# Kernel tuning notes

Measured on AMD Instinct MI355X. Metric: run time of the kernel, lower is better.

Reference implementation:

```python
import jax, jax.numpy as jnp
import numpy as np

N_GRAPHS = 128
N_NODES = 512
N = N_GRAPHS * N_NODES      # 65536 total nodes
E = 524288                  # edges (avg degree 8)
F_IN = 4                    # num_features
EMB = 4                     # embedding_dim
HEADS = 4
GDIM = 16                   # GATConv_dim
D = GDIM * HEADS            # 64 = d_model
NHEAD = 2                   # heads // 2
FF = 64                     # ff_hid_dim
OUT = 64                    # output_dim
N_GAT_REST = 3              # gat_layers - 1


def setup_inputs() -> dict:
    key = jax.random.key(0)
    ks = iter(jax.random.split(key, 64))
    def nrm(shape, fan_in):
        return jax.random.normal(next(ks), shape, jnp.float32) / np.float32(np.sqrt(fan_in))
    inp = {}
    inp['x'] = jax.random.normal(next(ks), (N, F_IN), jnp.float32)
    inp['edge_index'] = jax.random.randint(next(ks), (2, E), 0, N, dtype=jnp.int32)
    inp['batch'] = jnp.repeat(jnp.arange(N_GRAPHS, dtype=jnp.int32), N_NODES)
    # feature_fc
    inp['Wf'] = nrm((F_IN, EMB), F_IN); inp['bf'] = jnp.zeros((EMB,), jnp.float32)
    # input GATConv (EMB -> HEADS*GDIM)
    inp['gW0'] = nrm((EMB, HEADS * GDIM), EMB)
    inp['aS0'] = nrm((HEADS, GDIM), GDIM); inp['aD0'] = nrm((HEADS, GDIM), GDIM)
    inp['gb0'] = jnp.zeros((D,), jnp.float32)
    # remaining 3 GATConv layers (D -> HEADS*GDIM), stacked
    inp['gW'] = nrm((N_GAT_REST, D, HEADS * GDIM), D)
    inp['aS'] = nrm((N_GAT_REST, HEADS, GDIM), GDIM); inp['aD'] = nrm((N_GAT_REST, HEADS, GDIM), GDIM)
    inp['gb'] = jnp.zeros((N_GAT_REST, D), jnp.float32)
    # decoder layer: self-attn, cross-attn, layernorms, FFN
    for p in ['sWq','sWk','sWv','sWo','cWq','cWk','cWv','cWo']:
        inp[p] = nrm((D, D), D)
    for p in ['sbq','sbk','sbv','sbo','cbq','cbk','cbv','cbo']:
        inp[p] = jnp.zeros((D,), jnp.float32)
    for g, b in [('ln1g','ln1b'), ('ln2g','ln2b'), ('ln3g','ln3b')]:
        inp[g] = jnp.ones((D,), jnp.float32); inp[b] = jnp.zeros((D,), jnp.float32)
    inp['ffW1'] = nrm((D, FF), D); inp['ffb1'] = jnp.zeros((FF,), jnp.float32)
    inp['ffW2'] = nrm((FF, D), FF); inp['ffb2'] = jnp.zeros((D,), jnp.float32)
    inp['fcW'] = nrm((D, OUT), D); inp['fcb'] = jnp.zeros((OUT,), jnp.float32)
    return inp


def _gat(h_in, src, dst, W, a_s, a_d, b):
    # PyG GATConv, concat=True, negative_slope=0.2, self-loops already in (src,dst)
    h = (h_in @ W).reshape(N, HEADS, GDIM)
    es = jnp.einsum('nho,ho->nh', h, a_s)   # [N,H]
    ed = jnp.einsum('nho,ho->nh', h, a_d)
    e = jax.nn.leaky_relu(es[src] + ed[dst], 0.2)          # [E',H]
    m = jax.ops.segment_max(e, dst, num_segments=N)        # segment softmax over dst
    w = jnp.exp(e - m[dst])
    s = jax.ops.segment_sum(w, dst, num_segments=N)
    alpha = w / (s[dst] + 1e-16)
    out = jax.ops.segment_sum(h[src] * alpha[..., None], dst, num_segments=N)
    return out.reshape(N, D) + b


def _mha(q, kv, Wq, bq, Wk, bk, Wv, bv, Wo, bo):
    B, S, Dm = q.shape
    hd = Dm // NHEAD
    Q = (q @ Wq + bq).reshape(B, S, NHEAD, hd)
    K = (kv @ Wk + bk).reshape(B, S, NHEAD, hd)
    V = (kv @ Wv + bv).reshape(B, S, NHEAD, hd)
    a = jax.nn.softmax(jnp.einsum('bqhd,bkhd->bhqk', Q, K) / jnp.sqrt(jnp.float32(hd)), axis=-1)
    o = jnp.einsum('bhqk,bkhd->bqhd', a, V).reshape(B, S, Dm)
    return o @ Wo + bo


def _ln(x, g, b):
    m = x.mean(-1, keepdims=True)
    v = ((x - m) ** 2).mean(-1, keepdims=True)
    return (x - m) / jnp.sqrt(v + 1e-5) * g + b


def reference(x, edge_index, batch, Wf, bf, gW0, aS0, aD0, gb0, gW, aS, aD, gb,
              sWq, sWk, sWv, sWo, cWq, cWk, cWv, cWo,
              sbq, sbk, sbv, sbo, cbq, cbk, cbv, cbo,
              ln1g, ln1b, ln2g, ln2b, ln3g, ln3b,
              ffW1, ffb1, ffW2, ffb2, fcW, fcb):
    loops = jnp.arange(N, dtype=edge_index.dtype)
    src = jnp.concatenate([edge_index[0], loops])
    dst = jnp.concatenate([edge_index[1], loops])
    h = x @ Wf + bf
    h = jax.nn.leaky_relu(_gat(h, src, dst, gW0, aS0, aD0, gb0), 0.01)
    for i in range(N_GAT_REST):
        h = jax.nn.leaky_relu(_gat(h, src, dst, gW[i], aS[i], aD[i], gb[i]), 0.01)
    t = h.reshape(N_GRAPHS, N_NODES, D)
    # one transformer decoder layer, post-norm, memory = layer input
    mem = t
    t = _ln(t + _mha(t, t, sWq, sbq, sWk, sbk, sWv, sbv, sWo, sbo), ln1g, ln1b)
    t = _ln(t + _mha(t, mem, cWq, cbq, cWk, cbk, cWv, cbv, cWo, cbo), ln2g, ln2b)
    t = _ln(t + (jax.nn.relu(t @ ffW1 + ffb1) @ ffW2 + ffb2), ln3g, ln3b)
    h = t.reshape(N, D)
    pooled = jax.ops.segment_sum(h, batch, num_segments=N_GRAPHS) / jnp.float32(N_NODES)
    return pooled @ fcW + fcb
```

## Files before the change

### kernel.cpp

```cpp
#include <hip/hip_runtime.h>
#include <math.h>

#define NG 128
#define SEQ 512
#define NN 65536
#define EE 524288
#define DM 64
#define HSTR 80

typedef __attribute__((ext_vector_type(8))) short short8;
typedef __attribute__((ext_vector_type(4))) float f32x4;

__device__ __forceinline__ float lrelu(float x, float s){ return x > 0.f ? x : s*x; }

__device__ __forceinline__ unsigned short f2bf(float x){
  union { float f; unsigned u; } v; v.f = x;
  unsigned r = v.u + 0x7FFF + ((v.u>>16)&1);
  return (unsigned short)(r>>16);
}
__device__ __forceinline__ float bf2f(unsigned short x){
  union { unsigned u; float f; } v; v.u = ((unsigned)x)<<16;
  return v.f;
}

__global__ void k_count(const int* __restrict__ dst, int* __restrict__ deg){
  int e = blockIdx.x*256 + threadIdx.x;
  atomicAdd(&deg[dst[e]], 1);
}

__global__ void k_scan1(const int* __restrict__ deg, int* __restrict__ excl, int* __restrict__ bsums){
  __shared__ int sm[256];
  int tid = threadIdx.x;
  int i = blockIdx.x*256 + tid;
  int v = deg[i];
  sm[tid] = v;
  __syncthreads();
  int val = v;
  for (int off=1; off<256; off<<=1){
    int add = (tid>=off)? sm[tid-off] : 0;
    __syncthreads();
    val += add;
    sm[tid] = val;
    __syncthreads();
  }
  excl[i] = val - v;
  if (tid==255) bsums[blockIdx.x] = val;
}

__global__ void k_scan2(int* __restrict__ bsums){
  __shared__ int sm[256];
  int tid=threadIdx.x;
  int v = bsums[tid];
  sm[tid]=v;
  __syncthreads();
  int val=v;
  for (int off=1; off<256; off<<=1){
    int add = (tid>=off)? sm[tid-off]:0;
    __syncthreads();
    val += add;
    sm[tid]=val;
    __syncthreads();
  }
  bsums[tid] = val - v;
}

__global__ void k_scan3(const int* __restrict__ excl, const int* __restrict__ bsums,
                        int* __restrict__ rowp, int* __restrict__ cursor){
  int i = blockIdx.x*256 + threadIdx.x;
  int v = excl[i] + bsums[blockIdx.x];
  rowp[i]=v; cursor[i]=v;
  if (i==0) rowp[NN]=EE;
}

__global__ void k_fill(const int* __restrict__ src, const int* __restrict__ dst,
                       int* __restrict__ cursor, int* __restrict__ col){
  int e = blockIdx.x*256 + threadIdx.x;
  int d = dst[e];
  int p = atomicAdd(&cursor[d], 1);
  col[p] = src[e];
}

__global__ void __launch_bounds__(256) k_transform0(const float* __restrict__ x,
                            const float* __restrict__ Wf, const float* __restrict__ bf,
                            const float* __restrict__ gW0,
                            const float* __restrict__ aSp, const float* __restrict__ aDp,
                            unsigned short* __restrict__ hout, float* __restrict__ ed){
  __shared__ float inL[4][68];
  __shared__ float Wl[4][64];
  __shared__ float b0l[64];
  __shared__ float asl[64], adl[64];
  int tid = threadIdx.x;
  int n0 = blockIdx.x*64;
  if (tid < 64){
    asl[tid] = aSp[tid]; adl[tid] = aDp[tid];
    float b = 0.f;
    #pragma unroll
    for (int k=0;k<4;k++) b += bf[k]*gW0[k*64+tid];
    b0l[tid] = b;
  }
  {
    int i = tid>>6, j = tid&63;
    float s = 0.f;
    #pragma unroll
    for (int k=0;k<4;k++) s += Wf[i*4+k]*gW0[k*64+j];
    Wl[i][j] = s;
  }
  if (tid < 64){
    float4 v = *(const float4*)&x[(size_t)(n0+tid)*4];
    inL[0][tid]=v.x; inL[1][tid]=v.y; inL[2][tid]=v.z; inL[3][tid]=v.w;
  }
  __syncthreads();
  int i = tid>>4, j = tid&15;
  float acc[4][4];
  #pragma unroll
  for (int r=0;r<4;r++){
    #pragma unroll
    for (int c=0;c<4;c++) acc[r][c] = 0.f;
  }
  #pragma unroll
  for (int k=0;k<4;k++){
    float4 av = *(float4*)&inL[k][4*i];
    float4 bv = *(float4*)&Wl[k][4*j];
    float a_[4]={av.x,av.y,av.z,av.w}, b_[4]={bv.x,bv.y,bv.z,bv.w};
    #pragma unroll
    for (int r=0;r<4;r++){
      #pragma unroll
      for (int c=0;c<4;c++) acc[r][c] += a_[r]*b_[c];
    }
  }
  float4 asv = *(float4*)&asl[4*j];
  float4 adv = *(float4*)&adl[4*j];
  float4 bbv = *(float4*)&b0l[4*j];
  float bb[4] = {bbv.x, bbv.y, bbv.z, bbv.w};
  #pragma unroll
  for (int r=0;r<4;r++){
    float y0=acc[r][0]+bb[0], y1=acc[r][1]+bb[1], y2=acc[r][2]+bb[2], y3=acc[r][3]+bb[3];
    int node = n0 + 4*i + r;
    ushort4 hv;
    hv.x=f2bf(y0); hv.y=f2bf(y1); hv.z=f2bf(y2); hv.w=f2bf(y3);
    *(ushort4*)&hout[(size_t)node*HSTR + 4*j] = hv;
    float ps = y0*asv.x + y1*asv.y + y2*asv.z + y3*asv.w;
    float pd = y0*adv.x + y1*adv.y + y2*adv.z + y3*adv.w;
    ps += __shfl_xor(ps,1); ps += __shfl_xor(ps,2);
    pd += __shfl_xor(pd,1); pd += __shfl_xor(pd,2);
    if ((j&3)==0){
      *(float*)&hout[(size_t)node*HSTR + 64 + 2*(j>>2)] = ps;
      ed[(size_t)node*4 + (j>>2)] = pd;
    }
  }
}

__global__ void __launch_bounds__(256) k_transform_bf(const unsigned short* __restrict__ hin, const float* __restrict__ W,
                            const float* __restrict__ aSp, const float* __restrict__ aDp,
                            unsigned short* __restrict__ hout, float* __restrict__ ed){
  __shared__ float inL[64][68];
  __shared__ float Wl[64][64];
  __shared__ float asl[64], adl[64];
  int tid = threadIdx.x;
  int n0 = blockIdx.x*64;
  if (tid < 64){ asl[tid] = aSp[tid]; adl[tid] = aDp[tid]; }
  for (int idx=tid; idx<1024; idx+=256){
    int k = idx>>4, jj = (idx&15)<<2;
    *(float4*)&Wl[k][jj] = *(const float4*)&W[k*64+jj];
  }
  for (int idx=tid; idx<1024; idx+=256){
    int node = idx>>4, kk = (idx&15)<<2;
    ushort4 v = *(const ushort4*)&hin[(size_t)(n0+node)*64 + kk];
    inL[kk][node]=bf2f(v.x); inL[kk+1][node]=bf2f(v.y); inL[kk+2][node]=bf2f(v.z); inL[kk+3][node]=bf2f(v.w);
  }
  __syncthreads();
  int i = tid>>4, j = tid&15;
  float acc[4][4];
  #pragma unroll
  for (int r=0;r<4;r++){
    #pragma unroll
    for (int c=0;c<4;c++) acc[r][c] = 0.f;
  }
  #pragma unroll 4
  for (int k=0;k<64;k++){
    float4 av = *(float4*)&inL[k][4*i];
    float4 bv = *(float4*)&Wl[k][4*j];
    float a_[4]={av.x,av.y,av.z,av.w}, b_[4]={bv.x,bv.y,bv.z,bv.w};
    #pragma unroll
    for (int r=0;r<4;r++){
      #pragma unroll
      for (int c=0;c<4;c++) acc[r][c] += a_[r]*b_[c];
    }
  }
  float4 asv = *(float4*)&asl[4*j];
  float4 adv = *(float4*)&adl[4*j];
  #pragma unroll
  for (int r=0;r<4;r++){
    float y0=acc[r][0], y1=acc[r][1], y2=acc[r][2], y3=acc[r][3];
    int node = n0 + 4*i + r;
    ushort4 hv;
    hv.x=f2bf(y0); hv.y=f2bf(y1); hv.z=f2bf(y2); hv.w=f2bf(y3);
    *(ushort4*)&hout[(size_t)node*HSTR + 4*j] = hv;
    float ps = y0*asv.x + y1*asv.y + y2*asv.z + y3*asv.w;
    float pd = y0*adv.x + y1*adv.y + y2*adv.z + y3*adv.w;
    ps += __shfl_xor(ps,1); ps += __shfl_xor(ps,2);
    pd += __shfl_xor(pd,1); pd += __shfl_xor(pd,2);
    if ((j&3)==0){
      *(float*)&hout[(size_t)node*HSTR + 64 + 2*(j>>2)] = ps;
      ed[(size_t)node*4 + (j>>2)] = pd;
    }
  }
}

template<int BF16OUT>
__global__ void __launch_bounds__(256) k_aggregate(const unsigned short* __restrict__ h,
                            const float* __restrict__ ed, const int* __restrict__ rowp,
                            const int* __restrict__ col, const float* __restrict__ gb,
                            void* __restrict__ houtv){
  int tid = threadIdx.x;
  int n = blockIdx.x*4 + (tid>>6);
  int l = tid&63;
  int q = l>>4;
  int sl = l&15;
  int head = sl>>2;
  float edn = ed[(size_t)n*4 + head];
  float es_self = *(const float*)&h[(size_t)n*HSTR + 64 + 2*head];
  int beg = __builtin_amdgcn_readfirstlane(rowp[n]);
  int end = __builtin_amdgcn_readfirstlane(rowp[n+1]);
  float m = -1e30f, s = 0.f;
  float a0=0.f, a1=0.f, a2=0.f, a3=0.f;
  int i = beg;
  for (; i+8 <= end; i += 8){
    int c0=col[i], c1=col[i+1], c2=col[i+2], c3=col[i+3];
    int c4=col[i+4], c5=col[i+5], c6=col[i+6], c7=col[i+7];
    int t01 = (q&1)? c1 : c0;
    int t23 = (q&1)? c3 : c2;
    int sq0 = (q&2)? t23 : t01;
    int t45 = (q&1)? c5 : c4;
    int t67 = (q&1)? c7 : c6;
    int sq1 = (q&2)? t67 : t45;
    size_t b0r = (size_t)sq0*HSTR, b1r = (size_t)sq1*HSTR;
    ushort4 hv0 = *(const ushort4*)&h[b0r + 4*sl];
    ushort4 hv1 = *(const ushort4*)&h[b1r + 4*sl];
    float e0 = lrelu(*(const float*)&h[b0r + 64 + 2*head] + edn, 0.2f);
    float e1 = lrelu(*(const float*)&h[b1r + 64 + 2*head] + edn, 0.2f);
    float mx = fmaxf(e0, e1);
    if (__any(mx > m + 8.f)){
      float nm = fmaxf(m, mx);
      float c = __expf(m - nm);
      s*=c; a0*=c; a1*=c; a2*=c; a3*=c; m = nm;
    }
    float w0 = __expf(e0 - m);
    float w1 = __expf(e1 - m);
    s += w0 + w1;
    a0 += w0*bf2f(hv0.x) + w1*bf2f(hv1.x);
    a1 += w0*bf2f(hv0.y) + w1*bf2f(hv1.y);
    a2 += w0*bf2f(hv0.z) + w1*bf2f(hv1.z);
    a3 += w0*bf2f(hv0.w) + w1*bf2f(hv1.w);
  }
  if (i < end){
    int last = end-1;
    int i1=(i+1<last)?i+1:last, i2=(i+2<last)?i+2:last, i3=(i+3<last)?i+3:last;
    int i4=(i+4<last)?i+4:last, i5=(i+5<last)?i+5:last, i6=(i+6<last)?i+6:last;
    int c0=col[i], c1=col[i1], c2=col[i2], c3=col[i3];
    int c4=col[i4], c5=col[i5], c6=col[i6], c7=col[last];
    int t01 = (q&1)? c1 : c0;
    int t23 = (q&1)? c3 : c2;
    int sq0 = (q&2)? t23 : t01;
    int t45 = (q&1)? c5 : c4;
    int t67 = (q&1)? c7 : c6;
    int sq1 = (q&2)? t67 : t45;
    bool ac0 = (i + q) < end;
    bool ac1 = (i + 4 + q) < end;
    size_t b0r = (size_t)sq0*HSTR, b1r = (size_t)sq1*HSTR;
    ushort4 hv0 = *(const ushort4*)&h[b0r + 4*sl];
    ushort4 hv1 = *(const ushort4*)&h[b1r + 4*sl];
    float e0 = lrelu(*(const float*)&h[b0r + 64 + 2*head] + edn, 0.2f);
    float e1 = lrelu(*(const float*)&h[b1r + 64 + 2*head] + edn, 0.2f);
    if (!ac0) e0 = -1e30f;
    if (!ac1) e1 = -1e30f;
    float mx = fmaxf(e0, e1);
    if (__any(mx > m + 8.f)){
      float nm = fmaxf(m, mx);
      float c = __expf(m - nm);
      s*=c; a0*=c; a1*=c; a2*=c; a3*=c; m = nm;
    }
    float w0 = ac0 ? __expf(e0 - m) : 0.f;
    float w1 = ac1 ? __expf(e1 - m) : 0.f;
    s += w0 + w1;
    a0 += w0*bf2f(hv0.x) + w1*bf2f(hv1.x);
    a1 += w0*bf2f(hv0.y) + w1*bf2f(hv1.y);
    a2 += w0*bf2f(hv0.z) + w1*bf2f(hv1.z);
    a3 += w0*bf2f(hv0.w) + w1*bf2f(hv1.w);
  }
  #pragma unroll
  for (int off=16; off<=32; off<<=1){
    float m2 = __shfl_xor(m, off);
    float s2 = __shfl_xor(s, off);
    float b0 = __shfl_xor(a0, off);
    float b1 = __shfl_xor(a1, off);
    float b2 = __shfl_xor(a2, off);
    float b3 = __shfl_xor(a3, off);
    float nm = fmaxf(m, m2);
    float c1 = __expf(m - nm), c2 = __expf(m2 - nm);
    s  = s*c1  + s2*c2;
    a0 = a0*c1 + b0*c2;
    a1 = a1*c1 + b1*c2;
    a2 = a2*c1 + b2*c2;
    a3 = a3*c1 + b3*c2;
    m = nm;
  }
  {
    float e_self = lrelu(es_self + edn, 0.2f);
    float nm = fmaxf(m, e_self);
    float c = __expf(m - nm), cs = __expf(e_self - nm);
    ushort4 hs = *(const ushort4*)&h[(size_t)n*HSTR + 4*sl];
    s  = s*c  + cs;
    a0 = a0*c + cs*bf2f(hs.x);
    a1 = a1*c + cs*bf2f(hs.y);
    a2 = a2*c + cs*bf2f(hs.z);
    a3 = a3*c + cs*bf2f(hs.w);
  }
  if (q == 0){
    float inv = 1.f/(s + 1e-16f);
    float4 gv = *(const float4*)&gb[4*sl];
    float o0 = lrelu(a0*inv + gv.x, 0.01f);
    float o1 = lrelu(a1*inv + gv.y, 0.01f);
    float o2 = lrelu(a2*inv + gv.z, 0.01f);
    float o3 = lrelu(a3*inv + gv.w, 0.01f);
    if (BF16OUT){
      ushort4 hv; hv.x=f2bf(o0); hv.y=f2bf(o1); hv.z=f2bf(o2); hv.w=f2bf(o3);
      *(ushort4*)((unsigned short*)houtv + (size_t)n*64 + 4*sl) = hv;
    } else {
      *(float4*)((float*)houtv + (size_t)n*64 + 4*sl) = make_float4(o0,o1,o2,o3);
    }
  }
}

__global__ void __launch_bounds__(256) k_qkv3(const float* __restrict__ in0, const float* __restrict__ W0, const float* __restrict__ b0, unsigned short* __restrict__ o0,
                      const float* __restrict__ in1, const float* __restrict__ W1, const float* __restrict__ b1, unsigned short* __restrict__ o1,
                      const float* __restrict__ in2, const float* __restrict__ W2, const float* __restrict__ b2, unsigned short* __restrict__ o2,
                      float scl0){
  __shared__ float inL[64][68];
  __shared__ float Wl[64][64];
  int tid = threadIdx.x;
  int n0 = blockIdx.x*64;
  int i = tid>>4, j = tid&15;
  const float* ins[3] = {in0, in1, in2};
  const float* Ws[3] = {W0, W1, W2};
  const float* bs[3] = {b0, b1, b2};
  unsigned short* os[3] = {o0, o1, o2};
  const float* cur = nullptr;
  for (int w=0; w<3; w++){
    __syncthreads();
    if (ins[w] != cur){
      cur = ins[w];
      for (int idx=tid; idx<1024; idx+=256){
        int node = idx>>4, kk = (idx&15)<<2;
        float4 v = *(const float4*)&cur[(size_t)(n0+node)*64 + kk];
        inL[kk][node]=v.x; inL[kk+1][node]=v.y; inL[kk+2][node]=v.z; inL[kk+3][node]=v.w;
      }
    }
    for (int idx=tid; idx<1024; idx+=256){
      int k = idx>>4, jj = (idx&15)<<2;
      *(float4*)&Wl[k][jj] = *(const float4*)&Ws[w][k*64+jj];
    }
    __syncthreads();
    float acc[4][4];
    #pragma unroll
    for (int r=0;r<4;r++){
      #pragma unroll
      for (int c=0;c<4;c++) acc[r][c] = 0.f;
    }
    #pragma unroll 4
    for (int k=0;k<64;k++){
      float4 av = *(float4*)&inL[k][4*i];
      float4 bv = *(float4*)&Wl[k][4*j];
      float a_[4]={av.x,av.y,av.z,av.w}, b_[4]={bv.x,bv.y,bv.z,bv.w};
      #pragma unroll
      for (int r=0;r<4;r++){
        #pragma unroll
        for (int c=0;c<4;c++) acc[r][c] += a_[r]*b_[c];
      }
    }
    float4 bv = *(const float4*)&bs[w][4*j];
    float bb[4] = {bv.x, bv.y, bv.z, bv.w};
    float sc = (w==0) ? scl0 : 1.f;
    #pragma unroll
    for (int r=0;r<4;r++){
      ushort4 hv;
      hv.x = f2bf((acc[r][0]+bb[0])*sc);
      hv.y = f2bf((acc[r][1]+bb[1])*sc);
      hv.z = f2bf((acc[r][2]+bb[2])*sc);
      hv.w = f2bf((acc[r][3]+bb[3])*sc);
      *(ushort4*)&os[w][(size_t)(n0+4*i+r)*64 + 4*j] = hv;
    }
  }
}

__global__ void __launch_bounds__(256) k_resln_bf(const unsigned short* __restrict__ in, const float* __restrict__ W,
                               const float* __restrict__ b, const float* __restrict__ res,
                               const float* __restrict__ g, const float* __restrict__ bl,
                               float* __restrict__ out){
  __shared__ float inL[64][68];
  __shared__ float Wl[64][64];
  int tid = threadIdx.x;
  int n0 = blockIdx.x*64;
  for (int idx=tid; idx<1024; idx+=256){
    int k = idx>>4, jj = (idx&15)<<2;
    *(float4*)&Wl[k][jj] = *(const float4*)&W[k*64+jj];
  }
  for (int idx=tid; idx<1024; idx+=256){
    int node = idx>>4, kk = (idx&15)<<2;
    ushort4 v = *(const ushort4*)&in[(size_t)(n0+node)*64 + kk];
    inL[kk][node]=bf2f(v.x); inL[kk+1][node]=bf2f(v.y); inL[kk+2][node]=bf2f(v.z); inL[kk+3][node]=bf2f(v.w);
  }
  __syncthreads();
  int i = tid>>4, j = tid&15;
  float acc[4][4];
  #pragma unroll
  for (int r=0;r<4;r++){
    #pragma unroll
    for (int c=0;c<4;c++) acc[r][c] = 0.f;
  }
  #pragma unroll 4
  for (int k=0;k<64;k++){
    float4 av = *(float4*)&inL[k][4*i];
    float4 bv = *(float4*)&Wl[k][4*j];
    float a_[4]={av.x,av.y,av.z,av.w}, b_[4]={bv.x,bv.y,bv.z,bv.w};
    #pragma unroll
    for (int r=0;r<4;r++){
      #pragma unroll
      for (int c=0;c<4;c++) acc[r][c] += a_[r]*b_[c];
    }
  }
  float4 bv = *(const float4*)&b[4*j];
  float bb[4] = {bv.x, bv.y, bv.z, bv.w};
  float4 gv = *(const float4*)&g[4*j];
  float4 blv = *(const float4*)&bl[4*j];
  float gg[4] = {gv.x, gv.y, gv.z, gv.w};
  float bb2[4] = {blv.x, blv.y, blv.z, blv.w};
  #pragma unroll
  for (int r=0;r<4;r++){
    int node = n0 + 4*i + r;
    float4 rv = *(const float4*)&res[(size_t)node*64 + 4*j];
    float y[4] = {acc[r][0]+bb[0]+rv.x, acc[r][1]+bb[1]+rv.y,
                  acc[r][2]+bb[2]+rv.z, acc[r][3]+bb[3]+rv.w};
    float s = (y[0]+y[1]) + (y[2]+y[3]);
    s += __shfl_xor(s,1); s += __shfl_xor(s,2); s += __shfl_xor(s,4); s += __shfl_xor(s,8);
    float mean = s * (1.f/64.f);
    float d[4] = {y[0]-mean, y[1]-mean, y[2]-mean, y[3]-mean};
    float v = (d[0]*d[0]+d[1]*d[1]) + (d[2]*d[2]+d[3]*d[3]);
    v += __shfl_xor(v,1); v += __shfl_xor(v,2); v += __shfl_xor(v,4); v += __shfl_xor(v,8);
    float inv = rsqrtf(v*(1.f/64.f) + 1e-5f);
    *(float4*)&out[(size_t)node*64 + 4*j] =
      make_float4(d[0]*inv*gg[0]+bb2[0], d[1]*inv*gg[1]+bb2[1],
                  d[2]*inv*gg[2]+bb2[2], d[3]*inv*gg[3]+bb2[3]);
  }
}

__global__ void __launch_bounds__(256) k_ffn(const float* __restrict__ in,
                     const float* __restrict__ W1p, const float* __restrict__ b1p,
                     const float* __restrict__ W2p, const float* __restrict__ b2p,
                     const float* __restrict__ g, const float* __restrict__ bl,
                     float* __restrict__ out){
  __shared__ float inL[64][68];
  __shared__ float Wl[64][64];
  __shared__ float ffL[64][68];
  int tid = threadIdx.x;
  int n0 = blockIdx.x*64;
  for (int idx=tid; idx<1024; idx+=256){
    int k = idx>>4, jj = (idx&15)<<2;
    *(float4*)&Wl[k][jj] = *(const float4*)&W1p[k*64+jj];
  }
  for (int idx=tid; idx<1024; idx+=256){
    int node = idx>>4, kk = (idx&15)<<2;
    float4 v = *(const float4*)&in[(size_t)(n0+node)*64 + kk];
    inL[kk][node]=v.x; inL[kk+1][node]=v.y; inL[kk+2][node]=v.z; inL[kk+3][node]=v.w;
  }
  __syncthreads();
  int i = tid>>4, j = tid&15;
  float acc[4][4];
  #pragma unroll
  for (int r=0;r<4;r++){
    #pragma unroll
    for (int c=0;c<4;c++) acc[r][c] = 0.f;
  }
  #pragma unroll 4
  for (int k=0;k<64;k++){
    float4 av = *(float4*)&inL[k][4*i];
    float4 bv = *(float4*)&Wl[k][4*j];
    float a_[4]={av.x,av.y,av.z,av.w}, b_[4]={bv.x,bv.y,bv.z,bv.w};
    #pragma unroll
    for (int r=0;r<4;r++){
      #pragma unroll
      for (int c=0;c<4;c++) acc[r][c] += a_[r]*b_[c];
    }
  }
  float4 b1v = *(const float4*)&b1p[4*j];
  float bb1[4] = {b1v.x, b1v.y, b1v.z, b1v.w};
  #pragma unroll
  for (int r=0;r<4;r++){
    #pragma unroll
    for (int c=0;c<4;c++){
      ffL[4*j+c][4*i+r] = fmaxf(acc[r][c] + bb1[c], 0.f);
    }
  }
  __syncthreads();
  for (int idx=tid; idx<1024; idx+=256){
    int k = idx>>4, jj = (idx&15)<<2;
    *(float4*)&Wl[k][jj] = *(const float4*)&W2p[k*64+jj];
  }
  __syncthreads();
  #pragma unroll
  for (int r=0;r<4;r++){
    #pragma unroll
    for (int c=0;c<4;c++) acc[r][c] = 0.f;
  }
  #pragma unroll 4
  for (int k=0;k<64;k++){
    float4 av = *(float4*)&ffL[k][4*i];
    float4 bv = *(float4*)&Wl[k][4*j];
    float a_[4]={av.x,av.y,av.z,av.w}, b_[4]={bv.x,bv.y,bv.z,bv.w};
    #pragma unroll
    for (int r=0;r<4;r++){
      #pragma unroll
      for (int c=0;c<4;c++) acc[r][c] += a_[r]*b_[c];
    }
  }
  float4 b2v = *(const float4*)&b2p[4*j];
  float bb2v[4] = {b2v.x, b2v.y, b2v.z, b2v.w};
  float4 gv = *(const float4*)&g[4*j];
  float4 blv = *(const float4*)&bl[4*j];
  float gg[4] = {gv.x, gv.y, gv.z, gv.w};
  float bbl[4] = {blv.x, blv.y, blv.z, blv.w};
  #pragma unroll
  for (int r=0;r<4;r++){
    int node = n0 + 4*i + r;
    float y[4];
    #pragma unroll
    for (int c=0;c<4;c++) y[c] = acc[r][c] + bb2v[c] + inL[4*j+c][4*i+r];
    float s = (y[0]+y[1]) + (y[2]+y[3]);
    s += __shfl_xor(s,1); s += __shfl_xor(s,2); s += __shfl_xor(s,4); s += __shfl_xor(s,8);
    float mean = s * (1.f/64.f);
    float d[4] = {y[0]-mean, y[1]-mean, y[2]-mean, y[3]-mean};
    float v = (d[0]*d[0]+d[1]*d[1]) + (d[2]*d[2]+d[3]*d[3]);
    v += __shfl_xor(v,1); v += __shfl_xor(v,2); v += __shfl_xor(v,4); v += __shfl_xor(v,8);
    float inv = rsqrtf(v*(1.f/64.f) + 1e-5f);
    *(float4*)&out[(size_t)node*64 + 4*j] =
      make_float4(d[0]*inv*gg[0]+bbl[0], d[1]*inv*gg[1]+bbl[1],
                  d[2]*inv*gg[2]+bbl[2], d[3]*inv*gg[3]+bbl[3]);
  }
}

__global__ void __launch_bounds__(512, 4) k_attn(const unsigned short* __restrict__ Q, const unsigned short* __restrict__ K,
                      const unsigned short* __restrict__ V, unsigned short* __restrict__ Out){
  __shared__ char smem[40960];
  char* Ksm = smem;
  char* Vsm = smem + 16384;
  char* Psm = smem + 32768;

  int bid = blockIdx.x;
  int qh = bid & 1;
  int h  = (bid>>1) & 1;
  int b  = bid>>2;
  int tid = threadIdx.x;
  int wave = tid>>6;
  int l = tid & 63;
  int lq = l & 15;
  int g  = l >> 4;
  const size_t hb = (size_t)b*SEQ*64 + (size_t)h*32;
  const f32x4 zero = {0.f,0.f,0.f,0.f};

  int qbase = qh*256 + wave*32;
  short8 qf[2];
  f32x4 O[2][2];
  float m_[2], l_[2];
  #pragma unroll
  for (int qt=0; qt<2; qt++){
    qf[qt] = *(const short8*)(Q + hb + (size_t)(qbase + qt*16 + lq)*64 + g*8);
    O[qt][0] = zero; O[qt][1] = zero;
    m_[qt] = -1e30f; l_[qt] = 0.f;
  }

  char* Pw = Psm + wave*1024;

  for (int ph=0; ph<2; ph++){
    __syncthreads();
    #pragma unroll
    for (int it=0; it<2; it++){
      int i = tid + it*512;
      int row = i>>2, j = i&3;
      uint4 v = *(const uint4*)(K + hb + (size_t)(ph*256 + row)*64 + j*8);
      *(uint4*)(Ksm + row*64 + ((j*16) ^ (((row>>1)&3)<<4))) = v;
    }
    #pragma unroll
    for (int it=0; it<2; it++){
      int i = tid + it*512;
      int key = i>>2, j = i&3;
      uint4 vv = *(const uint4*)(V + hb + (size_t)(ph*256 + key)*64 + j*8);
      const unsigned short* vs = (const unsigned short*)&vv;
      #pragma unroll
      for (int c=0;c<8;c++){
        int d = j*8 + c;
        *(unsigned short*)(Vsm + d*512 + ((key*2) ^ ((d&7)<<4))) = vs[c];
      }
    }
    __syncthreads();
    for (int p=0; p<8; p++){
      int r0 = p*32 + lq, r1 = r0 + 16;
      short8 kf0 = *(short8*)(Ksm + r0*64 + ((g*16) ^ (((r0>>1)&3)<<4)));
      short8 kf1 = *(short8*)(Ksm + r1*64 + ((g*16) ^ (((r1>>1)&3)<<4)));
      int d0 = lq, d1 = lq + 16;
      short8 vt0 = *(short8*)(Vsm + d0*512 + ((p*64 + g*16) ^ ((d0&7)<<4)));
      short8 vt1 = *(short8*)(Vsm + d1*512 + ((p*64 + g*16) ^ ((d1&7)<<4)));
      int swzp = ((lq>>1)&3)<<4;
      #pragma unroll
      for (int qt=0; qt<2; qt++){
        f32x4 s0 = __builtin_amdgcn_mfma_f32_16x16x32_bf16(kf0, qf[qt], zero, 0,0,0);
        f32x4 s1 = __builtin_amdgcn_mfma_f32_16x16x32_bf16(kf1, qf[qt], zero, 0,0,0);
        float pmax = fmaxf(fmaxf(fmaxf(s0.x,s0.y),fmaxf(s0.z,s0.w)),
                           fmaxf(fmaxf(s1.x,s1.y),fmaxf(s1.z,s1.w)));
        pmax = fmaxf(pmax, __shfl_xor(pmax, 16));
        pmax = fmaxf(pmax, __shfl_xor(pmax, 32));
        float mn = fmaxf(m_[qt], pmax);
        float corr = __expf(m_[qt] - mn);
        m_[qt] = mn;
        float e0 = __expf(s0.x - mn), e1 = __expf(s0.y - mn);
        float e2 = __expf(s0.z - mn), e3 = __expf(s0.w - mn);
        float e4 = __expf(s1.x - mn), e5 = __expf(s1.y - mn);
        float e6 = __expf(s1.z - mn), e7 = __expf(s1.w - mn);
        l_[qt] = l_[qt]*corr + (((e0+e1)+(e2+e3)) + ((e4+e5)+(e6+e7)));
        O[qt][0] *= corr; O[qt][1] *= corr;
        uint2 w0, w1;
        w0.x = (unsigned)f2bf(e0) | ((unsigned)f2bf(e1)<<16);
        w0.y = (unsigned)f2bf(e2) | ((unsigned)f2bf(e3)<<16);
        w1.x = (unsigned)f2bf(e4) | ((unsigned)f2bf(e5)<<16);
        w1.y = (unsigned)f2bf(e6) | ((unsigned)f2bf(e7)<<16);
        *(uint2*)(Pw + lq*64 + ((g*8) ^ swzp)) = w0;
        *(uint2*)(Pw + lq*64 + ((32 + g*8) ^ swzp)) = w1;
        short8 pb = *(short8*)(Pw + lq*64 + ((g*16) ^ swzp));
        O[qt][0] = __builtin_amdgcn_mfma_f32_16x16x32_bf16(vt0, pb, O[qt][0], 0,0,0);
        O[qt][1] = __builtin_amdgcn_mfma_f32_16x16x32_bf16(vt1, pb, O[qt][1], 0,0,0);
      }
    }
  }
  #pragma unroll
  for (int qt=0; qt<2; qt++){
    float lt = l_[qt];
    lt += __shfl_xor(lt, 16);
    lt += __shfl_xor(lt, 32);
    float inv = 1.f/lt;
    unsigned short* op = Out + hb + (size_t)(qbase + qt*16 + lq)*64;
    ushort4 o0, o1;
    o0.x=f2bf(O[qt][0].x*inv); o0.y=f2bf(O[qt][0].y*inv); o0.z=f2bf(O[qt][0].z*inv); o0.w=f2bf(O[qt][0].w*inv);
    o1.x=f2bf(O[qt][1].x*inv); o1.y=f2bf(O[qt][1].y*inv); o1.z=f2bf(O[qt][1].z*inv); o1.w=f2bf(O[qt][1].w*inv);
    *(ushort4*)(op + g*4) = o0;
    *(ushort4*)(op + 16 + g*4) = o1;
  }
}

__global__ void __launch_bounds__(256) k_pool_fc(const float* __restrict__ t, const float* __restrict__ fcW,
                          const float* __restrict__ fcb, float* __restrict__ out){
  __shared__ float pl[4][64];
  __shared__ float pf[64];
  int b = blockIdx.x;
  int tid = threadIdx.x;
  int j = tid&63, seg = tid>>6;
  const float* basep = t + (size_t)b*SEQ*64;
  float s = 0.f;
  for (int si=seg*128; si<(seg+1)*128; si++) s += basep[(size_t)si*64 + j];
  pl[seg][j] = s;
  __syncthreads();
  if (tid < 64){
    pf[tid] = (pl[0][tid]+pl[1][tid]+pl[2][tid]+pl[3][tid]) * (1.f/512.f);
  }
  __syncthreads();
  if (tid < 64){
    float o = fcb[tid];
    for (int k=0;k<64;k++) o += pf[k]*fcW[k*64+tid];
    out[(size_t)b*64 + tid] = o;
  }
}

extern "C" void kernel_launch(void* const* d_in, const int* in_sizes, int n_in,
                              void* d_out, int out_size, void* d_ws, size_t ws_size,
                              hipStream_t stream) {
  const float* x    = (const float*)d_in[0];
  const int*   ei   = (const int*)d_in[1];
  const float* Wf   = (const float*)d_in[3];
  const float* bf   = (const float*)d_in[4];
  const float* gW0  = (const float*)d_in[5];
  const float* aS0  = (const float*)d_in[6];
  const float* aD0  = (const float*)d_in[7];
  const float* gb0  = (const float*)d_in[8];
  const float* gW   = (const float*)d_in[9];
  const float* aS   = (const float*)d_in[10];
  const float* aD   = (const float*)d_in[11];
  const float* gb   = (const float*)d_in[12];
  const float* sWq  = (const float*)d_in[13];
  const float* sWk  = (const float*)d_in[14];
  const float* sWv  = (const float*)d_in[15];
  const float* sWo  = (const float*)d_in[16];
  const float* cWq  = (const float*)d_in[17];
  const float* cWk  = (const float*)d_in[18];
  const float* cWv  = (const float*)d_in[19];
  const float* cWo  = (const float*)d_in[20];
  const float* sbq  = (const float*)d_in[21];
  const float* sbk  = (const float*)d_in[22];
  const float* sbv  = (const float*)d_in[23];
  const float* sbo  = (const float*)d_in[24];
  const float* cbq  = (const float*)d_in[25];
  const float* cbk  = (const float*)d_in[26];
  const float* cbv  = (const float*)d_in[27];
  const float* cbo  = (const float*)d_in[28];
  const float* ln1g = (const float*)d_in[29];
  const float* ln1b = (const float*)d_in[30];
  const float* ln2g = (const float*)d_in[31];
  const float* ln2b = (const float*)d_in[32];
  const float* ln3g = (const float*)d_in[33];
  const float* ln3b = (const float*)d_in[34];
  const float* ffW1 = (const float*)d_in[35];
  const float* ffb1 = (const float*)d_in[36];
  const float* ffW2 = (const float*)d_in[37];
  const float* ffb2 = (const float*)d_in[38];
  const float* fcW  = (const float*)d_in[39];
  const float* fcb  = (const float*)d_in[40];

  char* ws = (char*)d_ws;
  size_t off = 0;
  auto alloc = [&](size_t bytes) -> void* {
    void* p = ws + off;
    off += (bytes + 255) & ~(size_t)255;
    return p;
  };
  int* deg    = (int*)alloc(NN*sizeof(int));
  int* excl   = (int*)alloc(NN*sizeof(int));
  int* rowp   = (int*)alloc((NN+1)*sizeof(int));
  int* cursor = (int*)alloc(NN*sizeof(int));
  int* col    = (int*)alloc(EE*sizeof(int));
  int* bsums  = (int*)alloc(256*sizeof(int));
  float* ed   = (float*)alloc((size_t)NN*4*sizeof(float));
  unsigned short* Hb   = (unsigned short*)alloc((size_t)NN*HSTR*sizeof(unsigned short));
  unsigned short* Hagg = (unsigned short*)alloc((size_t)NN*64*sizeof(unsigned short));
  unsigned short* Qb = (unsigned short*)alloc((size_t)NN*64*sizeof(unsigned short));
  unsigned short* Kb = (unsigned short*)alloc((size_t)NN*64*sizeof(unsigned short));
  unsigned short* Vb = (unsigned short*)alloc((size_t)NN*64*sizeof(unsigned short));
  unsigned short* Ob = (unsigned short*)alloc((size_t)NN*64*sizeof(unsigned short));
  float* B1   = (float*)alloc((size_t)NN*64*sizeof(float));
  float* B2   = (float*)alloc((size_t)NN*64*sizeof(float));
  float* B5   = (float*)alloc((size_t)NN*64*sizeof(float));

  const int* e_src = ei;
  const int* e_dst = ei + EE;

  const float scale = 0.17677669529663687f;

  hipMemsetAsync(deg, 0, NN*sizeof(int), stream);
  k_count<<<EE/256, 256, 0, stream>>>(e_dst, deg);
  k_scan1<<<NN/256, 256, 0, stream>>>(deg, excl, bsums);
  k_scan2<<<1, 256, 0, stream>>>(bsums);
  k_scan3<<<NN/256, 256, 0, stream>>>(excl, bsums, rowp, cursor);
  k_fill<<<EE/256, 256, 0, stream>>>(e_src, e_dst, cursor, col);

  k_transform0<<<NN/64, 256, 0, stream>>>(x, Wf, bf, gW0, aS0, aD0, Hb, ed);
  k_aggregate<1><<<NN/4, 256, 0, stream>>>(Hb, ed, rowp, col, gb0, Hagg);
  k_transform_bf<<<NN/64, 256, 0, stream>>>(Hagg, gW+0*4096, aS+0*64, aD+0*64, Hb, ed);
  k_aggregate<1><<<NN/4, 256, 0, stream>>>(Hb, ed, rowp, col, gb+0*64, Hagg);
  k_transform_bf<<<NN/64, 256, 0, stream>>>(Hagg, gW+1*4096, aS+1*64, aD+1*64, Hb, ed);
  k_aggregate<1><<<NN/4, 256, 0, stream>>>(Hb, ed, rowp, col, gb+1*64, Hagg);
  k_transform_bf<<<NN/64, 256, 0, stream>>>(Hagg, gW+2*4096, aS+2*64, aD+2*64, Hb, ed);
  k_aggregate<0><<<NN/4, 256, 0, stream>>>(Hb, ed, rowp, col, gb+2*64, B2);

  k_qkv3<<<NN/64, 256, 0, stream>>>(B2, sWq, sbq, Qb, B2, sWk, sbk, Kb, B2, sWv, sbv, Vb, scale);
  k_attn<<<NG*2*2, 512, 0, stream>>>(Qb, Kb, Vb, Ob);
  k_resln_bf<<<NN/64, 256, 0, stream>>>(Ob, sWo, sbo, B2, ln1g, ln1b, B5);

  k_qkv3<<<NN/64, 256, 0, stream>>>(B5, cWq, cbq, Qb, B2, cWk, cbk, Kb, B2, cWv, cbv, Vb, scale);
  k_attn<<<NG*2*2, 512, 0, stream>>>(Qb, Kb, Vb, Ob);
  k_resln_bf<<<NN/64, 256, 0, stream>>>(Ob, cWo, cbo, B5, ln2g, ln2b, B2);

  k_ffn<<<NN/64, 256, 0, stream>>>(B2, ffW1, ffb1, ffW2, ffb2, ln3g, ln3b, B1);

  k_pool_fc<<<NG, 256, 0, stream>>>(B1, fcW, fcb, (float*)d_out);
}
```

Measured before the change: 412.1 us.

## Fuse attention with output projection, residual and layernorm per half-graph block

Merges the attention kernel and the output-projection plus residual-LayerNorm kernel into one. Each block now covers both heads for 256 query rows, so the normalized attention output is staged in shared memory and multiplied by Wo there instead of being written to and re-read from global memory. This removes the Ob buffer round trip and one launch per attention stage. In exchange the grid halves to 256 blocks, shared memory per block grows, and the launch-bounds occupancy hint is dropped, which may reduce parallelism on a large GPU.

```diff
diff --git a/kernel.cpp b/kernel.cpp
--- a/kernel.cpp
+++ b/kernel.cpp
@@ -393,67 +393,6 @@
   }
 }
 
-__global__ void __launch_bounds__(256) k_resln_bf(const unsigned short* __restrict__ in, const float* __restrict__ W,
-                               const float* __restrict__ b, const float* __restrict__ res,
-                               const float* __restrict__ g, const float* __restrict__ bl,
-                               float* __restrict__ out){
-  __shared__ float inL[64][68];
-  __shared__ float Wl[64][64];
-  int tid = threadIdx.x;
-  int n0 = blockIdx.x*64;
-  for (int idx=tid; idx<1024; idx+=256){
-    int k = idx>>4, jj = (idx&15)<<2;
-    *(float4*)&Wl[k][jj] = *(const float4*)&W[k*64+jj];
-  }
-  for (int idx=tid; idx<1024; idx+=256){
-    int node = idx>>4, kk = (idx&15)<<2;
-    ushort4 v = *(const ushort4*)&in[(size_t)(n0+node)*64 + kk];
-    inL[kk][node]=bf2f(v.x); inL[kk+1][node]=bf2f(v.y); inL[kk+2][node]=bf2f(v.z); inL[kk+3][node]=bf2f(v.w);
-  }
-  __syncthreads();
-  int i = tid>>4, j = tid&15;
-  float acc[4][4];
-  #pragma unroll
-  for (int r=0;r<4;r++){
-    #pragma unroll
-    for (int c=0;c<4;c++) acc[r][c] = 0.f;
-  }
-  #pragma unroll 4
-  for (int k=0;k<64;k++){
-    float4 av = *(float4*)&inL[k][4*i];
-    float4 bv = *(float4*)&Wl[k][4*j];
-    float a_[4]={av.x,av.y,av.z,av.w}, b_[4]={bv.x,bv.y,bv.z,bv.w};
-    #pragma unroll
-    for (int r=0;r<4;r++){
-      #pragma unroll
-      for (int c=0;c<4;c++) acc[r][c] += a_[r]*b_[c];
-    }
-  }
-  float4 bv = *(const float4*)&b[4*j];
-  float bb[4] = {bv.x, bv.y, bv.z, bv.w};
-  float4 gv = *(const float4*)&g[4*j];
-  float4 blv = *(const float4*)&bl[4*j];
-  float gg[4] = {gv.x, gv.y, gv.z, gv.w};
-  float bb2[4] = {blv.x, blv.y, blv.z, blv.w};
-  #pragma unroll
-  for (int r=0;r<4;r++){
-    int node = n0 + 4*i + r;
-    float4 rv = *(const float4*)&res[(size_t)node*64 + 4*j];
-    float y[4] = {acc[r][0]+bb[0]+rv.x, acc[r][1]+bb[1]+rv.y,
-                  acc[r][2]+bb[2]+rv.z, acc[r][3]+bb[3]+rv.w};
-    float s = (y[0]+y[1]) + (y[2]+y[3]);
-    s += __shfl_xor(s,1); s += __shfl_xor(s,2); s += __shfl_xor(s,4); s += __shfl_xor(s,8);
-    float mean = s * (1.f/64.f);
-    float d[4] = {y[0]-mean, y[1]-mean, y[2]-mean, y[3]-mean};
-    float v = (d[0]*d[0]+d[1]*d[1]) + (d[2]*d[2]+d[3]*d[3]);
-    v += __shfl_xor(v,1); v += __shfl_xor(v,2); v += __shfl_xor(v,4); v += __shfl_xor(v,8);
-    float inv = rsqrtf(v*(1.f/64.f) + 1e-5f);
-    *(float4*)&out[(size_t)node*64 + 4*j] =
-      make_float4(d[0]*inv*gg[0]+bb2[0], d[1]*inv*gg[1]+bb2[1],
-                  d[2]*inv*gg[2]+bb2[2], d[3]*inv*gg[3]+bb2[3]);
-  }
-}
-
 __global__ void __launch_bounds__(256) k_ffn(const float* __restrict__ in,
                      const float* __restrict__ W1p, const float* __restrict__ b1p,
                      const float* __restrict__ W2p, const float* __restrict__ b2p,
@@ -548,70 +487,74 @@
   }
 }
 
-__global__ void __launch_bounds__(512, 4) k_attn(const unsigned short* __restrict__ Q, const unsigned short* __restrict__ K,
-                      const unsigned short* __restrict__ V, unsigned short* __restrict__ Out){
-  __shared__ char smem[40960];
+__global__ void __launch_bounds__(512) k_attn_fused(const unsigned short* __restrict__ Q, const unsigned short* __restrict__ K,
+                      const unsigned short* __restrict__ V,
+                      const float* __restrict__ Wo, const float* __restrict__ bo,
+                      const float* __restrict__ res, const float* __restrict__ g, const float* __restrict__ bl,
+                      float* __restrict__ out){
+  __shared__ __align__(16) char smem[52224];
   char* Ksm = smem;
   char* Vsm = smem + 16384;
   char* Psm = smem + 32768;
 
   int bid = blockIdx.x;
   int qh = bid & 1;
-  int h  = (bid>>1) & 1;
-  int b  = bid>>2;
+  int b  = bid >> 1;
   int tid = threadIdx.x;
   int wave = tid>>6;
   int l = tid & 63;
   int lq = l & 15;
-  int g  = l >> 4;
-  const size_t hb = (size_t)b*SEQ*64 + (size_t)h*32;
+  int g4 = l >> 4;
+  int head = wave & 1;
+  int qg = wave >> 1;
+  const size_t gb = (size_t)b*SEQ*64;
+  const int hoff = head*32;
   const f32x4 zero = {0.f,0.f,0.f,0.f};
 
-  int qbase = qh*256 + wave*32;
-  short8 qf[2];
-  f32x4 O[2][2];
-  float m_[2], l_[2];
-  #pragma unroll
-  for (int qt=0; qt<2; qt++){
-    qf[qt] = *(const short8*)(Q + hb + (size_t)(qbase + qt*16 + lq)*64 + g*8);
+  int qrow0 = qh*256 + qg*64;
+  short8 qf[4];
+  f32x4 O[4][2];
+  float m_[4], l_[4];
+  #pragma unroll
+  for (int qt=0; qt<4; qt++){
+    qf[qt] = *(const short8*)(Q + gb + (size_t)(qrow0 + qt*16 + lq)*64 + hoff + g4*8);
     O[qt][0] = zero; O[qt][1] = zero;
     m_[qt] = -1e30f; l_[qt] = 0.f;
   }
-
   char* Pw = Psm + wave*1024;
 
-  for (int ph=0; ph<2; ph++){
+  for (int ph=0; ph<4; ph++){
     __syncthreads();
     #pragma unroll
     for (int it=0; it<2; it++){
-      int i = tid + it*512;
-      int row = i>>2, j = i&3;
-      uint4 v = *(const uint4*)(K + hb + (size_t)(ph*256 + row)*64 + j*8);
-      *(uint4*)(Ksm + row*64 + ((j*16) ^ (((row>>1)&3)<<4))) = v;
+      int idx = tid + it*512;
+      int row = idx>>3, gr = idx&7;
+      uint4 v = *(const uint4*)(K + gb + (size_t)(ph*128 + row)*64 + gr*8);
+      *(uint4*)(Ksm + row*128 + ((gr*16) ^ ((row&7)<<4))) = v;
     }
     #pragma unroll
     for (int it=0; it<2; it++){
-      int i = tid + it*512;
-      int key = i>>2, j = i&3;
-      uint4 vv = *(const uint4*)(V + hb + (size_t)(ph*256 + key)*64 + j*8);
+      int idx = tid + it*512;
+      int key = idx>>3, gr = idx&7;
+      uint4 vv = *(const uint4*)(V + gb + (size_t)(ph*128 + key)*64 + gr*8);
       const unsigned short* vs = (const unsigned short*)&vv;
       #pragma unroll
       for (int c=0;c<8;c++){
-        int d = j*8 + c;
-        *(unsigned short*)(Vsm + d*512 + ((key*2) ^ ((d&7)<<4))) = vs[c];
+        int d = gr*8 + c;
+        *(unsigned short*)(Vsm + d*256 + ((key*2) ^ ((d&7)<<4))) = vs[c];
       }
     }
     __syncthreads();
-    for (int p=0; p<8; p++){
+    for (int p=0; p<4; p++){
       int r0 = p*32 + lq, r1 = r0 + 16;
-      short8 kf0 = *(short8*)(Ksm + r0*64 + ((g*16) ^ (((r0>>1)&3)<<4)));
-      short8 kf1 = *(short8*)(Ksm + r1*64 + ((g*16) ^ (((r1>>1)&3)<<4)));
-      int d0 = lq, d1 = lq + 16;
-      short8 vt0 = *(short8*)(Vsm + d0*512 + ((p*64 + g*16) ^ ((d0&7)<<4)));
-      short8 vt1 = *(short8*)(Vsm + d1*512 + ((p*64 + g*16) ^ ((d1&7)<<4)));
+      short8 kf0 = *(short8*)(Ksm + r0*128 + ((hoff*2 + g4*16) ^ ((r0&7)<<4)));
+      short8 kf1 = *(short8*)(Ksm + r1*128 + ((hoff*2 + g4*16) ^ ((r1&7)<<4)));
+      int d0 = hoff + lq, d1 = hoff + lq + 16;
+      short8 vt0 = *(short8*)(Vsm + d0*256 + ((p*64 + g4*16) ^ ((d0&7)<<4)));
+      short8 vt1 = *(short8*)(Vsm + d1*256 + ((p*64 + g4*16) ^ ((d1&7)<<4)));
       int swzp = ((lq>>1)&3)<<4;
       #pragma unroll
-      for (int qt=0; qt<2; qt++){
+      for (int qt=0; qt<4; qt++){
         f32x4 s0 = __builtin_amdgcn_mfma_f32_16x16x32_bf16(kf0, qf[qt], zero, 0,0,0);
         f32x4 s1 = __builtin_amdgcn_mfma_f32_16x16x32_bf16(kf1, qf[qt], zero, 0,0,0);
         float pmax = fmaxf(fmaxf(fmaxf(s0.x,s0.y),fmaxf(s0.z,s0.w)),
@@ -632,26 +575,77 @@
         w0.y = (unsigned)f2bf(e2) | ((unsigned)f2bf(e3)<<16);
         w1.x = (unsigned)f2bf(e4) | ((unsigned)f2bf(e5)<<16);
         w1.y = (unsigned)f2bf(e6) | ((unsigned)f2bf(e7)<<16);
-        *(uint2*)(Pw + lq*64 + ((g*8) ^ swzp)) = w0;
-        *(uint2*)(Pw + lq*64 + ((32 + g*8) ^ swzp)) = w1;
-        short8 pb = *(short8*)(Pw + lq*64 + ((g*16) ^ swzp));
+        *(uint2*)(Pw + lq*64 + ((g4*8) ^ swzp)) = w0;
+        *(uint2*)(Pw + lq*64 + ((32 + g4*8) ^ swzp)) = w1;
+        short8 pb = *(short8*)(Pw + lq*64 + ((g4*16) ^ swzp));
         O[qt][0] = __builtin_amdgcn_mfma_f32_16x16x32_bf16(vt0, pb, O[qt][0], 0,0,0);
         O[qt][1] = __builtin_amdgcn_mfma_f32_16x16x32_bf16(vt1, pb, O[qt][1], 0,0,0);
       }
     }
   }
-  #pragma unroll
-  for (int qt=0; qt<2; qt++){
+  __syncthreads();
+  unsigned short* OT = (unsigned short*)smem;
+  float* WoL = (float*)(smem + 34816);
+  #pragma unroll
+  for (int qt=0; qt<4; qt++){
     float lt = l_[qt];
     lt += __shfl_xor(lt, 16);
     lt += __shfl_xor(lt, 32);
     float inv = 1.f/lt;
-    unsigned short* op = Out + hb + (size_t)(qbase + qt*16 + lq)*64;
-    ushort4 o0, o1;
-    o0.x=f2bf(O[qt][0].x*inv); o0.y=f2bf(O[qt][0].y*inv); o0.z=f2bf(O[qt][0].z*inv); o0.w=f2bf(O[qt][0].w*inv);
-    o1.x=f2bf(O[qt][1].x*inv); o1.y=f2bf(O[qt][1].y*inv); o1.z=f2bf(O[qt][1].z*inv); o1.w=f2bf(O[qt][1].w*inv);
-    *(ushort4*)(op + g*4) = o0;
-    *(ushort4*)(op + 16 + g*4) = o1;
+    int row = qg*64 + qt*16 + lq;
+    #pragma unroll
+    for (int c=0;c<4;c++){
+      OT[(hoff + g4*4 + c)*272 + row]      = f2bf(O[qt][0][c]*inv);
+      OT[(hoff + 16 + g4*4 + c)*272 + row] = f2bf(O[qt][1][c]*inv);
+    }
+  }
+  for (int idx=tid; idx<1024; idx+=512){
+    int k = idx>>4, jj = (idx&15)<<2;
+    *(float4*)&WoL[k*64+jj] = *(const float4*)&Wo[k*64+jj];
+  }
+  __syncthreads();
+  int i = tid>>4, j = tid&15;
+  float acc[8][4];
+  #pragma unroll
+  for (int r=0;r<8;r++){
+    #pragma unroll
+    for (int c=0;c<4;c++) acc[r][c] = 0.f;
+  }
+  #pragma unroll 4
+  for (int k=0;k<64;k++){
+    short8 av = *(short8*)&OT[k*272 + 8*i];
+    float4 bv = *(float4*)&WoL[k*64 + 4*j];
+    float b_[4]={bv.x,bv.y,bv.z,bv.w};
+    #pragma unroll
+    for (int r=0;r<8;r++){
+      float a = bf2f((unsigned short)av[r]);
+      #pragma unroll
+      for (int c=0;c<4;c++) acc[r][c] += a*b_[c];
+    }
+  }
+  float4 bov = *(const float4*)&bo[4*j];
+  float4 gv = *(const float4*)&g[4*j];
+  float4 blv = *(const float4*)&bl[4*j];
+  float bb[4] = {bov.x, bov.y, bov.z, bov.w};
+  float gg[4] = {gv.x, gv.y, gv.z, gv.w};
+  float bbl[4] = {blv.x, blv.y, blv.z, blv.w};
+  #pragma unroll
+  for (int r=0;r<8;r++){
+    int row = 8*i + r;
+    int node = b*SEQ + qh*256 + row;
+    float4 rv = *(const float4*)&res[(size_t)node*64 + 4*j];
+    float y[4] = {acc[r][0]+bb[0]+rv.x, acc[r][1]+bb[1]+rv.y,
+                  acc[r][2]+bb[2]+rv.z, acc[r][3]+bb[3]+rv.w};
+    float s = (y[0]+y[1]) + (y[2]+y[3]);
+    s += __shfl_xor(s,1); s += __shfl_xor(s,2); s += __shfl_xor(s,4); s += __shfl_xor(s,8);
+    float mean = s * (1.f/64.f);
+    float d[4] = {y[0]-mean, y[1]-mean, y[2]-mean, y[3]-mean};
+    float v = (d[0]*d[0]+d[1]*d[1]) + (d[2]*d[2]+d[3]*d[3]);
+    v += __shfl_xor(v,1); v += __shfl_xor(v,2); v += __shfl_xor(v,4); v += __shfl_xor(v,8);
+    float inv = rsqrtf(v*(1.f/64.f) + 1e-5f);
+    *(float4*)&out[(size_t)node*64 + 4*j] =
+      make_float4(d[0]*inv*gg[0]+bbl[0], d[1]*inv*gg[1]+bbl[1],
+                  d[2]*inv*gg[2]+bbl[2], d[3]*inv*gg[3]+bbl[3]);
   }
 }
 
@@ -741,7 +735,6 @@
   unsigned short* Qb = (unsigned short*)alloc((size_t)NN*64*sizeof(unsigned short));
   unsigned short* Kb = (unsigned short*)alloc((size_t)NN*64*sizeof(unsigned short));
   unsigned short* Vb = (unsigned short*)alloc((size_t)NN*64*sizeof(unsigned short));
-  unsigned short* Ob = (unsigned short*)alloc((size_t)NN*64*sizeof(unsigned short));
   float* B1   = (float*)alloc((size_t)NN*64*sizeof(float));
   float* B2   = (float*)alloc((size_t)NN*64*sizeof(float));
   float* B5   = (float*)alloc((size_t)NN*64*sizeof(float));
@@ -768,12 +761,10 @@
   k_aggregate<0><<<NN/4, 256, 0, stream>>>(Hb, ed, rowp, col, gb+2*64, B2);
 
   k_qkv3<<<NN/64, 256, 0, stream>>>(B2, sWq, sbq, Qb, B2, sWk, sbk, Kb, B2, sWv, sbv, Vb, scale);
-  k_attn<<<NG*2*2, 512, 0, stream>>>(Qb, Kb, Vb, Ob);
-  k_resln_bf<<<NN/64, 256, 0, stream>>>(Ob, sWo, sbo, B2, ln1g, ln1b, B5);
+  k_attn_fused<<<NG*2, 512, 0, stream>>>(Qb, Kb, Vb, sWo, sbo, B2, ln1g, ln1b, B5);
 
   k_qkv3<<<NN/64, 256, 0, stream>>>(B5, cWq, cbq, Qb, B2, cWk, cbk, Kb, B2, cWv, cbv, Vb, scale);
-  k_attn<<<NG*2*2, 512, 0, stream>>>(Qb, Kb, Vb, Ob);
-  k_resln_bf<<<NN/64, 256, 0, stream>>>(Ob, cWo, cbo, B5, ln2g, ln2b, B2);
+  k_attn_fused<<<NG*2, 512, 0, stream>>>(Qb, Kb, Vb, cWo, cbo, B5, ln2g, ln2b, B2);
 
   k_ffn<<<NN/64, 256, 0, stream>>>(B2, ffW1, ffb1, ffW2, ffb2, ln3g, ln3b, B1);
 
```

Result: no change. 408.0 us (-1.0%).
